# Optimization experiments

Measured on AMD Instinct MI355X. Metric: run time of the kernel, lower is better.

## Reference

```python
import jax, jax.numpy as jnp
import numpy as np

DIM = 1024
NHEAD = 16
HEAD_DIM = DIM // NHEAD


def setup_inputs() -> dict:
    key = jax.random.key(0)
    k_x, k_wqkv, k_bqkv, k_wp, k_bp = jax.random.split(key, 5)
    scale = 1.0 / np.sqrt(DIM)
    return {
        "x": jax.random.normal(k_x, (4, 2048, DIM), dtype=jnp.float32),
        "w_qkv": jax.random.uniform(k_wqkv, (DIM, 3 * DIM), minval=-scale, maxval=scale, dtype=jnp.float32),
        "b_qkv": jax.random.uniform(k_bqkv, (3 * DIM,), minval=-scale, maxval=scale, dtype=jnp.float32),
        "w_proj": jax.random.uniform(k_wp, (DIM, DIM), minval=-scale, maxval=scale, dtype=jnp.float32),
        "b_proj": jax.random.uniform(k_bp, (DIM,), minval=-scale, maxval=scale, dtype=jnp.float32),
    }


def reference(x, w_qkv, b_qkv, w_proj, b_proj):
    B, N, D = x.shape
    # qkv projection: [B,N,3D] -> [3,B,H,N,hd]
    qkv = x @ w_qkv + b_qkv
    qkv = qkv.reshape(B, N, 3, NHEAD, HEAD_DIM).transpose(2, 0, 3, 1, 4)
    q, k, v = qkv[0], qkv[1], qkv[2]
    # naive full attention: scores [B,H,N,N]
    attn = jnp.einsum("bhqd,bhkd->bhqk", q, k) / jnp.sqrt(jnp.float32(HEAD_DIM))
    attn = jax.nn.softmax(attn, axis=-1)
    out = jnp.einsum("bhqk,bhkd->bhqd", attn, v)  # [B,H,N,hd]
    out = out.transpose(0, 2, 1, 3).reshape(B, N, D)
    return out @ w_proj + b_proj
```

## Files before the change

kernel.cpp:

```cpp
#include <hip/hip_runtime.h>
#include <math.h>

#define DIM     1024
#define NHEAD   16
#define HD      64
#define BATCH   4
#define SEQ     2048
#define MTOT    (BATCH * SEQ)
#define QKV_N   (3 * DIM)

typedef __attribute__((ext_vector_type(8))) short bf16x8;
typedef __attribute__((ext_vector_type(4))) float f32x4;
typedef unsigned int u32;
typedef unsigned short u16;

__device__ __forceinline__ u16 f2bf(float f) {
    u32 u = __float_as_uint(f);
    return (u16)((u + 0x7fffu + ((u >> 16) & 1u)) >> 16);
}

__device__ __forceinline__ float exp2_fast(float x) {
    float r; asm("v_exp_f32 %0, %1" : "=v"(r) : "v"(x)); return r;
}

__device__ __forceinline__ u32 cvtpk_bf16(float lo, float hi) {
    u32 r; asm("v_cvt_pk_bf16_f32 %0, %1, %2" : "=v"(r) : "v"(lo), "v"(hi));
    return r;
}

__device__ __forceinline__ void gload_lds16(const u16* g, u16* l) {
    __builtin_amdgcn_global_load_lds((const __attribute__((address_space(1))) u32*)g,
                                     (__attribute__((address_space(3))) u32*)l, 16, 0, 0);
}

__global__ __launch_bounds__(256) void prep(
    const float* __restrict__ x,  u16* __restrict__ xb,
    const float* __restrict__ wq, u16* __restrict__ wqt,
    const float* __restrict__ wp, u16* __restrict__ wpt)
{
    const int b = blockIdx.x;
    if (b < 8192) {
        const int i = (b * 256 + threadIdx.x) * 4;
        const float4 v = *(const float4*)&x[i];
        ushort4 o;
        o.x = f2bf(v.x); o.y = f2bf(v.y); o.z = f2bf(v.z); o.w = f2bf(v.w);
        *(ushort4*)&xb[i] = o;
        return;
    }
    __shared__ float Ls[64][65];
    int i = b - 8192;
    const float* W; u16* Wt; int N;
    if (i < 768) { W = wq; Wt = wqt; N = QKV_N; }
    else         { i -= 768; W = wp; Wt = wpt; N = DIM; }
    const int k0 = (i & 15) * 64, n0 = (i >> 4) * 64;
    const int t = threadIdx.x;
    const int r = t >> 4, c4 = (t & 15) << 2;
    #pragma unroll
    for (int j = 0; j < 4; ++j) {
        const float4 v = *(const float4*)&W[(size_t)(k0 + r + j * 16) * N + n0 + c4];
        Ls[r + j * 16][c4 + 0] = v.x; Ls[r + j * 16][c4 + 1] = v.y;
        Ls[r + j * 16][c4 + 2] = v.z; Ls[r + j * 16][c4 + 3] = v.w;
    }
    __syncthreads();
    #pragma unroll
    for (int j = 0; j < 4; ++j) {
        const int nr = r + j * 16;
        ushort4 o;
        o.x = f2bf(Ls[c4 + 0][nr]); o.y = f2bf(Ls[c4 + 1][nr]);
        o.z = f2bf(Ls[c4 + 2][nr]); o.w = f2bf(Ls[c4 + 3][nr]);
        *(ushort4*)&Wt[(size_t)(n0 + nr) * DIM + k0 + c4] = o;
    }
}

#define GEMM_STAGE(buf, kof, Aptr, Bptr)                                       \
    _Pragma("unroll") for (int i = 0; i < 2; ++i) {                            \
        const int row = w * 32 + i * 16 + (lane >> 2);                         \
        const int slot = (lane & 3) ^ ((row >> 1) & 3);                        \
        gload_lds16(&Aptr[(size_t)(m0 + row) * DIM + (kof) + slot * 8],        \
                    &As[buf][(w * 32 + i * 16) * 32]);                         \
        gload_lds16(&Bptr[(size_t)(n0 + row) * DIM + (kof) + slot * 8],        \
                    &Bs[buf][(w * 32 + i * 16) * 32]);                         \
    }

#define GEMM_MAINLOOP(Aptr, Bptr)                                              \
    __shared__ __align__(16) u16 As[2][128 * 32];                              \
    __shared__ __align__(16) u16 Bs[2][128 * 32];                              \
    const int t = threadIdx.x;                                                 \
    const int lane = t & 63, w = t >> 6;                                       \
    const int n0 = blockIdx.x * 128;                                           \
    const int m0 = blockIdx.y * 128;                                           \
    const int wm = (w & 1) * 64, wn = (w >> 1) * 64;                           \
    const int g = lane >> 4, li = lane & 15;                                   \
    f32x4 acc[4][4];                                                           \
    _Pragma("unroll") for (int mt = 0; mt < 4; ++mt)                           \
        _Pragma("unroll") for (int nt = 0; nt < 4; ++nt)                       \
            acc[mt][nt] = (f32x4){0.f, 0.f, 0.f, 0.f};                         \
    GEMM_STAGE(0, 0, Aptr, Bptr)                                               \
    __syncthreads();                                                           \
    int cur = 0;                                                               \
    for (int k0 = 0; k0 < DIM; k0 += 32) {                                     \
        if (k0 + 32 < DIM) { GEMM_STAGE(cur ^ 1, k0 + 32, Aptr, Bptr) }        \
        bf16x8 a[4], b[4];                                                     \
        _Pragma("unroll") for (int mt = 0; mt < 4; ++mt) {                     \
            const int row = wm + mt * 16 + li;                                 \
            const int slot = g ^ ((row >> 1) & 3);                             \
            a[mt] = *(const bf16x8*)&As[cur][row * 32 + slot * 8];             \
        }                                                                      \
        _Pragma("unroll") for (int nt = 0; nt < 4; ++nt) {                     \
            const int row = wn + nt * 16 + li;                                 \
            const int slot = g ^ ((row >> 1) & 3);                             \
            b[nt] = *(const bf16x8*)&Bs[cur][row * 32 + slot * 8];             \
        }                                                                      \
        _Pragma("unroll") for (int mt = 0; mt < 4; ++mt)                       \
            _Pragma("unroll") for (int nt = 0; nt < 4; ++nt)                   \
                acc[mt][nt] = __builtin_amdgcn_mfma_f32_16x16x32_bf16(         \
                    a[mt], b[nt], acc[mt][nt], 0, 0, 0);                       \
        __syncthreads();                                                       \
        cur ^= 1;                                                              \
    }

#define QSCALE 0.18033688011112042f
__global__ __launch_bounds__(256) void gemm_qkv(
    const u16* __restrict__ A, const u16* __restrict__ Bt,
    const float* __restrict__ bias,
    u16* __restrict__ qo, u16* __restrict__ ko, u16* __restrict__ vo)
{
    GEMM_MAINLOOP(A, Bt)
    #pragma unroll
    for (int nt = 0; nt < 4; ++nt) {
        const int n = n0 + wn + nt * 16 + li;
        const int which = n >> 10;
        const int head  = (n >> 6) & 15;
        const int hd    = n & 63;
        u16* dst = (which == 0) ? qo : (which == 1) ? ko : vo;
        const float scale = (which == 0) ? QSCALE : 1.0f;
        const float bv = bias[n];
        #pragma unroll
        for (int mt = 0; mt < 4; ++mt) {
            #pragma unroll
            for (int r = 0; r < 4; ++r) {
                const int m = m0 + wm + mt * 16 + g * 4 + r;
                const int bb = m >> 11, tok = m & 2047;
                dst[((size_t)(bb * NHEAD + head) * SEQ + tok) * HD + hd] =
                    f2bf((acc[mt][nt][r] + bv) * scale);
            }
        }
    }
}

__global__ __launch_bounds__(256) void gemm_proj(
    const u16* __restrict__ A, const u16* __restrict__ Bt,
    const float* __restrict__ bias, float* __restrict__ out)
{
    GEMM_MAINLOOP(A, Bt)
    #pragma unroll
    for (int nt = 0; nt < 4; ++nt) {
        const int n = n0 + wn + nt * 16 + li;
        const float bv = bias[n];
        #pragma unroll
        for (int mt = 0; mt < 4; ++mt) {
            #pragma unroll
            for (int r = 0; r < 4; ++r) {
                const int m = m0 + wm + mt * 16 + g * 4 + r;
                out[(size_t)m * DIM + n] = acc[mt][nt][r] + bv;
            }
        }
    }
}

#define LSTR 72
#define NKT  (SEQ / 64)
__global__ __launch_bounds__(512) void attn_mfma(
    const u16* __restrict__ q, const u16* __restrict__ k,
    const u16* __restrict__ v, u16* __restrict__ ao)
{
    __shared__ __align__(16) u16 Ks[2][64 * LSTR];
    __shared__ __align__(16) u16 Vt[2][64 * LSTR];

    const int t = threadIdx.x;
    const int lane = t & 63, w = t >> 6;
    const int g = lane >> 4, li = lane & 15;
    const int q0 = blockIdx.x * 256;
    const int bh = blockIdx.y;
    const size_t base = (size_t)bh * SEQ * HD;

    bf16x8 qf[2][2];
    #pragma unroll
    for (int h = 0; h < 2; ++h) {
        const size_t qrow = base + (size_t)(q0 + w * 32 + h * 16 + li) * HD;
        qf[h][0] = *(const bf16x8*)&q[qrow + g * 8];
        qf[h][1] = *(const bf16x8*)&q[qrow + 32 + g * 8];
    }

    float lsum[2] = {0.f, 0.f};
    f32x4 oacc[2][4];
    #pragma unroll
    for (int h = 0; h < 2; ++h)
        #pragma unroll
        for (int nt = 0; nt < 4; ++nt) oacc[h][nt] = (f32x4){0.f, 0.f, 0.f, 0.f};

    const int kk = t >> 3;
    const int kh = (t & 7) << 3;
    const int kperm = (kk & 32) | (((kk >> 2) & 3) << 3)
                    | (((kk >> 4) & 1) << 2) | (kk & 3);
    const int vkp = (t & 31) << 1;
    const int vh0 = (t >> 5) << 2;

    bf16x8 rk;
    ushort4 rv0, rv1;
    rk  = *(const bf16x8*)&k[base + (size_t)kperm * HD + kh];
    rv0 = *(const ushort4*)&v[base + (size_t)vkp * HD + vh0];
    rv1 = *(const ushort4*)&v[base + (size_t)(vkp + 1) * HD + vh0];
    {
        u16* Kn = Ks[0]; u16* Vn = Vt[0];
        *(bf16x8*)&Kn[kk * LSTR + kh] = rk;
        const u16 a0[4] = {rv0.x, rv0.y, rv0.z, rv0.w};
        const u16 b0[4] = {rv1.x, rv1.y, rv1.z, rv1.w};
        #pragma unroll
        for (int i = 0; i < 4; ++i)
            *(u32*)&Vn[(vh0 + i) * LSTR + vkp] = (u32)a0[i] | ((u32)b0[i] << 16);
    }
    __syncthreads();

    int cur = 0;
    for (int kt = 0; kt < NKT; ++kt) {
        const bool more = (kt + 1 < NKT);
        if (more) {
            const size_t kb = base + (size_t)(kt + 1) * 64 * HD;
            rk  = *(const bf16x8*)&k[kb + (size_t)kperm * HD + kh];
            rv0 = *(const ushort4*)&v[kb + (size_t)vkp * HD + vh0];
            rv1 = *(const ushort4*)&v[kb + (size_t)(vkp + 1) * HD + vh0];
        }
        const u16* Kc = Ks[cur];
        const u16* Vc = Vt[cur];

        f32x4 s[2][4];
        __builtin_amdgcn_s_setprio(1);
        #pragma unroll
        for (int nt = 0; nt < 4; ++nt) {
            const bf16x8 kf0 = *(const bf16x8*)&Kc[(nt * 16 + li) * LSTR + g * 8];
            const bf16x8 kf1 = *(const bf16x8*)&Kc[(nt * 16 + li) * LSTR + 32 + g * 8];
            #pragma unroll
            for (int h = 0; h < 2; ++h) {
                f32x4 c = (f32x4){0.f, 0.f, 0.f, 0.f};
                c = __builtin_amdgcn_mfma_f32_16x16x32_bf16(kf0, qf[h][0], c, 0, 0, 0);
                c = __builtin_amdgcn_mfma_f32_16x16x32_bf16(kf1, qf[h][1], c, 0, 0, 0);
                s[h][nt] = c;
            }
        }
        __builtin_amdgcn_s_setprio(0);

        bf16x8 pb[2][2];
        #pragma unroll
        for (int h = 0; h < 2; ++h) {
            float rs = 0.f;
            #pragma unroll
            for (int nt = 0; nt < 4; ++nt)
                #pragma unroll
                for (int r = 0; r < 4; ++r) {
                    const float p = exp2_fast(s[h][nt][r]);
                    s[h][nt][r] = p;
                    rs += p;
                }
            lsum[h] += rs;
            #pragma unroll
            for (int ks = 0; ks < 2; ++ks) {
                union { u32 u[4]; bf16x8 v8; } uu;
                uu.u[0] = cvtpk_bf16(s[h][2 * ks][0],     s[h][2 * ks][1]);
                uu.u[1] = cvtpk_bf16(s[h][2 * ks][2],     s[h][2 * ks][3]);
                uu.u[2] = cvtpk_bf16(s[h][2 * ks + 1][0], s[h][2 * ks + 1][1]);
                uu.u[3] = cvtpk_bf16(s[h][2 * ks + 1][2], s[h][2 * ks + 1][3]);
                pb[h][ks] = uu.v8;
            }
        }

        __builtin_amdgcn_s_setprio(1);
        #pragma unroll
        for (int ks = 0; ks < 2; ++ks) {
            #pragma unroll
            for (int nt = 0; nt < 4; ++nt) {
                const bf16x8 vb = *(const bf16x8*)&Vc[(nt * 16 + li) * LSTR + ks * 32 + g * 8];
                #pragma unroll
                for (int h = 0; h < 2; ++h)
                    oacc[h][nt] = __builtin_amdgcn_mfma_f32_16x16x32_bf16(
                        vb, pb[h][ks], oacc[h][nt], 0, 0, 0);
            }
        }
        __builtin_amdgcn_s_setprio(0);

        if (more) {
            u16* Kn = Ks[cur ^ 1]; u16* Vn = Vt[cur ^ 1];
            *(bf16x8*)&Kn[kk * LSTR + kh] = rk;
            const u16 a0[4] = {rv0.x, rv0.y, rv0.z, rv0.w};
            const u16 b0[4] = {rv1.x, rv1.y, rv1.z, rv1.w};
            #pragma unroll
            for (int i = 0; i < 4; ++i)
                *(u32*)&Vn[(vh0 + i) * LSTR + vkp] = (u32)a0[i] | ((u32)b0[i] << 16);
        }
        __syncthreads();
        cur ^= 1;
    }

    const int bb = bh >> 4, hh = bh & 15;
    #pragma unroll
    for (int h = 0; h < 2; ++h) {
        float lf = lsum[h];
        lf += __shfl_xor(lf, 16);
        lf += __shfl_xor(lf, 32);
        const float inv = 1.0f / lf;
        const int tok = q0 + w * 32 + h * 16 + li;
        u16* dst = &ao[(size_t)(bb * SEQ + tok) * DIM + hh * HD];
        #pragma unroll
        for (int nt = 0; nt < 4; ++nt) {
            const u32 p0 = cvtpk_bf16(oacc[h][nt][0] * inv, oacc[h][nt][1] * inv);
            const u32 p1 = cvtpk_bf16(oacc[h][nt][2] * inv, oacc[h][nt][3] * inv);
            *(u32*)&dst[nt * 16 + g * 4]     = p0;
            *(u32*)&dst[nt * 16 + g * 4 + 2] = p1;
        }
    }
}

extern "C" void kernel_launch(void* const* d_in, const int* in_sizes, int n_in,
                              void* d_out, int out_size, void* d_ws, size_t ws_size,
                              hipStream_t stream)
{
    const float* x      = (const float*)d_in[0];
    const float* w_qkv  = (const float*)d_in[1];
    const float* b_qkv  = (const float*)d_in[2];
    const float* w_proj = (const float*)d_in[3];
    const float* b_proj = (const float*)d_in[4];
    float* out = (float*)d_out;

    u16* xb  = (u16*)d_ws;
    u16* wqt = xb  + (size_t)MTOT * DIM;
    u16* wpt = wqt + (size_t)QKV_N * DIM;
    u16* qb  = wpt + (size_t)DIM * DIM;
    u16* kb  = qb  + (size_t)MTOT * DIM;
    u16* vb  = kb  + (size_t)MTOT * DIM;
    u16* aob = vb  + (size_t)MTOT * DIM;

    prep<<<8192 + 768 + 256, 256, 0, stream>>>(x, xb, w_qkv, wqt, w_proj, wpt);
    gemm_qkv<<<dim3(QKV_N / 128, MTOT / 128), 256, 0, stream>>>(xb, wqt, b_qkv, qb, kb, vb);
    attn_mfma<<<dim3(SEQ / 256, BATCH * NHEAD), 512, 0, stream>>>(qb, kb, vb, aob);
    gemm_proj<<<dim3(DIM / 128, MTOT / 128), 256, 0, stream>>>(aob, wpt, b_proj, out);
}
```

Before: 193.1 us.

## Fuse fp32-to-bf16 conversion of x into QKV GEMM and remap attention block order

Removes the separate pass that converts x to bf16. The QKV GEMM now loads fp32 rows of x into registers, converts them with v_cvt_pk_bf16_f32 and writes them into LDS after the compute step, which saves writing and re-reading the bf16 copy of x. The cost is that GEMM reads twice as many A bytes, and each of the 24 column blocks re-reads them. The A loads are also now register-staged instead of going directly global-to-LDS. The attention kernel also permutes its block index so that consecutive blocks spread across different batch-head pairs, which changes cache locality.

```diff
diff --git a/kernel.cpp b/kernel.cpp
--- a/kernel.cpp
+++ b/kernel.cpp
@@ -34,21 +34,11 @@
 }
 
 __global__ __launch_bounds__(256) void prep(
-    const float* __restrict__ x,  u16* __restrict__ xb,
     const float* __restrict__ wq, u16* __restrict__ wqt,
     const float* __restrict__ wp, u16* __restrict__ wpt)
 {
-    const int b = blockIdx.x;
-    if (b < 8192) {
-        const int i = (b * 256 + threadIdx.x) * 4;
-        const float4 v = *(const float4*)&x[i];
-        ushort4 o;
-        o.x = f2bf(v.x); o.y = f2bf(v.y); o.z = f2bf(v.z); o.w = f2bf(v.w);
-        *(ushort4*)&xb[i] = o;
-        return;
-    }
     __shared__ float Ls[64][65];
-    int i = b - 8192;
+    int i = blockIdx.x;
     const float* W; u16* Wt; int N;
     if (i < 768) { W = wq; Wt = wqt; N = QKV_N; }
     else         { i -= 768; W = wp; Wt = wpt; N = DIM; }
@@ -72,19 +62,43 @@
     }
 }
 
-#define GEMM_STAGE(buf, kof, Aptr, Bptr)                                       \
+#define GEMM_STAGE_B(buf, kof, Bptr)                                           \
+    _Pragma("unroll") for (int i = 0; i < 2; ++i) {                            \
+        const int row = w * 32 + i * 16 + (lane >> 2);                         \
+        const int slot = (lane & 3) ^ ((row >> 1) & 3);                        \
+        gload_lds16(&Bptr[(size_t)(n0 + row) * DIM + (kof) + slot * 8],        \
+                    &Bs[buf][(w * 32 + i * 16) * 32]);                         \
+    }
+
+#define GEMM_STAGE_A16(buf, kof, Aptr)                                         \
     _Pragma("unroll") for (int i = 0; i < 2; ++i) {                            \
         const int row = w * 32 + i * 16 + (lane >> 2);                         \
         const int slot = (lane & 3) ^ ((row >> 1) & 3);                        \
         gload_lds16(&Aptr[(size_t)(m0 + row) * DIM + (kof) + slot * 8],        \
                     &As[buf][(w * 32 + i * 16) * 32]);                         \
-        gload_lds16(&Bptr[(size_t)(n0 + row) * DIM + (kof) + slot * 8],        \
-                    &Bs[buf][(w * 32 + i * 16) * 32]);                         \
-    }
-
-#define GEMM_MAINLOOP(Aptr, Bptr)                                              \
-    __shared__ __align__(16) u16 As[2][128 * 32];                              \
-    __shared__ __align__(16) u16 Bs[2][128 * 32];                              \
+    }
+
+#define GEMM_LOADA32(kof, Aptr)                                                \
+    _Pragma("unroll") for (int i = 0; i < 2; ++i) {                            \
+        const int row = w * 32 + i * 16 + (lane >> 2);                         \
+        const int slot = (lane & 3) ^ ((row >> 1) & 3);                        \
+        const float* ap = &Aptr[(size_t)(m0 + row) * DIM + (kof) + slot * 8];  \
+        ra[i][0] = *(const float4*)ap;                                         \
+        ra[i][1] = *(const float4*)(ap + 4);                                   \
+    }
+
+#define GEMM_WRITEA32(buf)                                                     \
+    _Pragma("unroll") for (int i = 0; i < 2; ++i) {                            \
+        const int row = w * 32 + i * 16 + (lane >> 2);                         \
+        u32 pk4[4];                                                            \
+        pk4[0] = cvtpk_bf16(ra[i][0].x, ra[i][0].y);                           \
+        pk4[1] = cvtpk_bf16(ra[i][0].z, ra[i][0].w);                           \
+        pk4[2] = cvtpk_bf16(ra[i][1].x, ra[i][1].y);                           \
+        pk4[3] = cvtpk_bf16(ra[i][1].z, ra[i][1].w);                           \
+        *(uint4*)&As[buf][row * 32 + (lane & 3) * 8] = *(uint4*)pk4;           \
+    }
+
+#define GEMM_PREAMBLE                                                          \
     const int t = threadIdx.x;                                                 \
     const int lane = t & 63, w = t >> 6;                                       \
     const int n0 = blockIdx.x * 128;                                           \
@@ -94,38 +108,73 @@
     f32x4 acc[4][4];                                                           \
     _Pragma("unroll") for (int mt = 0; mt < 4; ++mt)                           \
         _Pragma("unroll") for (int nt = 0; nt < 4; ++nt)                       \
-            acc[mt][nt] = (f32x4){0.f, 0.f, 0.f, 0.f};                         \
-    GEMM_STAGE(0, 0, Aptr, Bptr)                                               \
-    __syncthreads();                                                           \
-    int cur = 0;                                                               \
-    for (int k0 = 0; k0 < DIM; k0 += 32) {                                     \
-        if (k0 + 32 < DIM) { GEMM_STAGE(cur ^ 1, k0 + 32, Aptr, Bptr) }        \
+            acc[mt][nt] = (f32x4){0.f, 0.f, 0.f, 0.f};
+
+#define GEMM_COMPUTE(buf)                                                      \
+    {                                                                          \
         bf16x8 a[4], b[4];                                                     \
         _Pragma("unroll") for (int mt = 0; mt < 4; ++mt) {                     \
             const int row = wm + mt * 16 + li;                                 \
             const int slot = g ^ ((row >> 1) & 3);                             \
-            a[mt] = *(const bf16x8*)&As[cur][row * 32 + slot * 8];             \
+            a[mt] = *(const bf16x8*)&As[buf][row * 32 + slot * 8];             \
         }                                                                      \
         _Pragma("unroll") for (int nt = 0; nt < 4; ++nt) {                     \
             const int row = wn + nt * 16 + li;                                 \
             const int slot = g ^ ((row >> 1) & 3);                             \
-            b[nt] = *(const bf16x8*)&Bs[cur][row * 32 + slot * 8];             \
+            b[nt] = *(const bf16x8*)&Bs[buf][row * 32 + slot * 8];             \
         }                                                                      \
         _Pragma("unroll") for (int mt = 0; mt < 4; ++mt)                       \
             _Pragma("unroll") for (int nt = 0; nt < 4; ++nt)                   \
                 acc[mt][nt] = __builtin_amdgcn_mfma_f32_16x16x32_bf16(         \
                     a[mt], b[nt], acc[mt][nt], 0, 0, 0);                       \
+    }
+
+#define GEMM_MAINLOOP(Aptr, Bptr)                                              \
+    __shared__ __align__(16) u16 As[2][128 * 32];                              \
+    __shared__ __align__(16) u16 Bs[2][128 * 32];                              \
+    GEMM_PREAMBLE                                                              \
+    GEMM_STAGE_A16(0, 0, Aptr)                                                 \
+    GEMM_STAGE_B(0, 0, Bptr)                                                   \
+    __syncthreads();                                                           \
+    int cur = 0;                                                               \
+    for (int k0 = 0; k0 < DIM; k0 += 32) {                                     \
+        if (k0 + 32 < DIM) {                                                   \
+            GEMM_STAGE_A16(cur ^ 1, k0 + 32, Aptr)                             \
+            GEMM_STAGE_B(cur ^ 1, k0 + 32, Bptr)                               \
+        }                                                                      \
+        GEMM_COMPUTE(cur)                                                      \
         __syncthreads();                                                       \
         cur ^= 1;                                                              \
     }
 
+#define GEMM_MAINLOOP_F32A(Aptr, Bptr)                                         \
+    __shared__ __align__(16) u16 As[2][128 * 32];                              \
+    __shared__ __align__(16) u16 Bs[2][128 * 32];                              \
+    GEMM_PREAMBLE                                                              \
+    float4 ra[2][2];                                                           \
+    GEMM_LOADA32(0, Aptr)                                                      \
+    GEMM_STAGE_B(0, 0, Bptr)                                                   \
+    GEMM_WRITEA32(0)                                                           \
+    __syncthreads();                                                           \
+    int cur = 0;                                                               \
+    for (int k0 = 0; k0 < DIM; k0 += 32) {                                     \
+        if (k0 + 32 < DIM) {                                                   \
+            GEMM_LOADA32(k0 + 32, Aptr)                                        \
+            GEMM_STAGE_B(cur ^ 1, k0 + 32, Bptr)                               \
+        }                                                                      \
+        GEMM_COMPUTE(cur)                                                      \
+        if (k0 + 32 < DIM) { GEMM_WRITEA32(cur ^ 1) }                          \
+        __syncthreads();                                                       \
+        cur ^= 1;                                                              \
+    }
+
 #define QSCALE 0.18033688011112042f
 __global__ __launch_bounds__(256) void gemm_qkv(
-    const u16* __restrict__ A, const u16* __restrict__ Bt,
+    const float* __restrict__ A, const u16* __restrict__ Bt,
     const float* __restrict__ bias,
     u16* __restrict__ qo, u16* __restrict__ ko, u16* __restrict__ vo)
 {
-    GEMM_MAINLOOP(A, Bt)
+    GEMM_MAINLOOP_F32A(A, Bt)
     #pragma unroll
     for (int nt = 0; nt < 4; ++nt) {
         const int n = n0 + wn + nt * 16 + li;
@@ -180,8 +229,11 @@
     const int t = threadIdx.x;
     const int lane = t & 63, w = t >> 6;
     const int g = lane >> 4, li = lane & 15;
-    const int q0 = blockIdx.x * 256;
-    const int bh = blockIdx.y;
+
+    int flat = blockIdx.y * 8 + blockIdx.x;
+    flat = (flat & 7) * 64 + (flat >> 3);
+    const int q0 = (flat & 7) * 256;
+    const int bh = flat >> 3;
     const size_t base = (size_t)bh * SEQ * HD;
 
     bf16x8 qf[2][2];
@@ -339,8 +391,8 @@
     u16* vb  = kb  + (size_t)MTOT * DIM;
     u16* aob = vb  + (size_t)MTOT * DIM;
 
-    prep<<<8192 + 768 + 256, 256, 0, stream>>>(x, xb, w_qkv, wqt, w_proj, wpt);
-    gemm_qkv<<<dim3(QKV_N / 128, MTOT / 128), 256, 0, stream>>>(xb, wqt, b_qkv, qb, kb, vb);
+    prep<<<1024, 256, 0, stream>>>(w_qkv, wqt, w_proj, wpt);
+    gemm_qkv<<<dim3(QKV_N / 128, MTOT / 128), 256, 0, stream>>>(x, wqt, b_qkv, qb, kb, vb);
     attn_mfma<<<dim3(SEQ / 256, BATCH * NHEAD), 512, 0, stream>>>(qb, kb, vb, aob);
     gemm_proj<<<dim3(DIM / 128, MTOT / 128), 256, 0, stream>>>(aob, wpt, b_proj, out);
 }
```

Result: no change. 195.4 us (+1.2%).
